# Performance work log

Measured on AMD Instinct MI355X. Metric: run time of the kernel, lower is better.

## Reference

```python
import jax, jax.numpy as jnp
import numpy as np

N_NODES = 32768
N_EDGES = 131072
BATCH = 512
SEQ_LEN = 1000
VOCAB = 26  # vocab_size=25 + 1 padding row
EMB = 128


def _bn(x, g, b):
    # BatchNorm1d forward with batch statistics (training-mode math), eps=1e-5
    m = x.mean(0)
    v = x.var(0)
    return g * (x - m) * jax.lax.rsqrt(v + 1e-5) + b


def _gcn(x, src, dst, W, b, n):
    deg = 1.0 + jax.ops.segment_sum(jnp.ones(src.shape[0], x.dtype), dst, num_segments=n)
    dis = jax.lax.rsqrt(deg)
    xw = x @ W
    msg = xw[src] * (dis[src] * dis[dst])[:, None]
    agg = jax.ops.segment_sum(msg, dst, num_segments=n) + xw * (dis * dis)[:, None]
    return agg + b


def _conv1d(x, k, b, pad):
    # x: [B, C_in, L], k: [C_out, C_in, K]
    y = jax.lax.conv_general_dilated(x, k, (1,), [(pad, pad)],
                                     dimension_numbers=('NCH', 'OIH', 'NCH'))
    return y + b[None, :, None]


def setup_inputs() -> dict:
    key = jax.random.key(0)
    ks = jax.random.split(key, 32)
    f = lambda i, shape, s=0.1: (jax.random.normal(ks[i], shape, dtype=jnp.float32) * s)
    inp = {
        'x': jax.random.normal(ks[0], (N_NODES, 5), dtype=jnp.float32),
        'edge_index': jax.random.randint(ks[1], (2, N_EDGES), 0, N_NODES, dtype=jnp.int32),
        'batch': jnp.sort(jax.random.randint(ks[2], (N_NODES,), 0, BATCH, dtype=jnp.int32)),
        'protein_seq': jax.random.randint(ks[3], (BATCH, SEQ_LEN), 0, VOCAB, dtype=jnp.int32),
        # GCN weights
        'W1': f(4, (5, 64)), 'b1': f(5, (64,)),
        'g1': jnp.ones((64,)), 'bt1': jnp.zeros((64,)),
        'W2': f(6, (64, 128)), 'b2': f(7, (128,)),
        'g2': jnp.ones((128,)), 'bt2': jnp.zeros((128,)),
        'W3': f(8, (128, 128)), 'b3': f(9, (128,)),
        'g3': jnp.ones((128,)), 'bt3': jnp.zeros((128,)),
        # protein embedding (row 0 = padding_idx, zeroed)
        'emb': f(10, (VOCAB, EMB)).at[0].set(0.0),
        # protein convs
        'ck1': f(11, (32, 128, 4)), 'cb1': f(12, (32,)),
        'ck2': f(13, (64, 32, 6)), 'cb2': f(14, (64,)),
        'ck3': f(15, (96, 64, 8)), 'cb3': f(16, (96,)),
        'fw1': f(17, (224, 512)), 'fb1': f(18, (512,)),
        'fw2': f(19, (512, 256)), 'fb2': f(20, (256,)),
        'fw3': f(21, (256, 1)), 'fb3': f(22, (1,)),
    }
    return inp


def reference(x, edge_index, batch, protein_seq,
              W1, b1, g1, bt1, W2, b2, g2, bt2, W3, b3, g3, bt3,
              emb, ck1, cb1, ck2, cb2, ck3, cb3,
              fw1, fb1, fw2, fb2, fw3, fb3):
    src, dst = edge_index[0], edge_index[1]
    relu = jax.nn.relu
    # Drug GNN encoder
    h = relu(_bn(_gcn(x, src, dst, W1, b1, N_NODES), g1, bt1))
    h = relu(_bn(_gcn(h, src, dst, W2, b2, N_NODES), g2, bt2))
    h = relu(_bn(_gcn(h, src, dst, W3, b3, N_NODES), g3, bt3))
    cnt = jax.ops.segment_sum(jnp.ones(N_NODES, h.dtype), batch, num_segments=BATCH)
    drug_emb = jax.ops.segment_sum(h, batch, num_segments=BATCH) / jnp.maximum(cnt, 1.0)[:, None]
    # Protein CNN encoder
    e = emb[protein_seq]                    # [B, L, 128]
    p = jnp.transpose(e, (0, 2, 1))         # [B, 128, L]
    p = relu(_conv1d(p, ck1, cb1, 1))       # [B, 32, 999]
    p = relu(_conv1d(p, ck2, cb2, 2))       # [B, 64, 998]
    p = relu(_conv1d(p, ck3, cb3, 3))       # [B, 96, 997]
    prot_emb = p.max(axis=2)                # [B, 96]
    c = jnp.concatenate([drug_emb, prot_emb], axis=1)  # [B, 224]
    c = relu(c @ fw1 + fb1)
    c = relu(c @ fw2 + fb2)
    out = (c @ fw3 + fb3)[:, 0]             # [B]
    return out
```

## Files before the change

### kernel.cpp

```cpp
#include <hip/hip_runtime.h>

#define NN 32768
#define NE 131072
#define NB 512
#define SL 1000

using bf16x8 = __attribute__((ext_vector_type(8))) short;
using f32x4  = __attribute__((ext_vector_type(4))) float;

static __device__ __forceinline__ unsigned short f2b(float f) {
  union { float f; unsigned u; } x; x.f = f;
  unsigned r = x.u + 0x7fffu + ((x.u >> 16) & 1u);
  return (unsigned short)(r >> 16);
}

static __device__ __forceinline__ void bn_from_raw(float sum, float ssq, float g, float b,
                                                   float& sc, float& sh) {
  float m = sum / 32768.f;
  float v = ssq / 32768.f - m * m;
  sc = g * rsqrtf(v + 1e-5f);
  sh = b - m * sc;
}

__global__ void k_degprep(const int* __restrict__ dst, int* __restrict__ degi,
                          const float* __restrict__ emb, const float* __restrict__ ck1,
                          const float* __restrict__ ck2, const float* __restrict__ ck3,
                          unsigned short* __restrict__ wt2, unsigned short* __restrict__ wt3,
                          float* __restrict__ e1) {
  int gid = blockIdx.x * 256 + threadIdx.x;
  atomicAdd(&degi[dst[gid]], 1);
  int idx = gid;
  if (idx < 12288) {
    int i = idx;
    int kt = i >> 11, co = (i >> 5) & 63, ci = i & 31;
    wt2[i] = f2b(ck2[co * 192 + ci * 6 + kt]);
  } else if (idx < 12288 + 49152) {
    int i = idx - 12288;
    int kt = i / 6144, co = (i >> 6) % 96, ci = i & 63;
    wt3[i] = f2b(ck3[co * 512 + ci * 8 + kt]);
  } else if (idx < 12288 + 49152 + 3328) {
    int i = idx - 61440;
    int t = i >> 7, kt = (i >> 5) & 3, co = i & 31;
    const float* er = emb + t * 128;
    float s = 0.f;
#pragma unroll 4
    for (int ci = 0; ci < 128; ++ci) s += er[ci] * ck1[co * 512 + ci * 4 + kt];
    e1[i] = s;
  }
}

__global__ void k_scan(const int* __restrict__ degi, int* __restrict__ base,
                       int* __restrict__ cursor, float* __restrict__ dis) {
  __shared__ int part[1024];
  int tid = threadIdx.x;
  int v[32];
  int s = 0;
  int lo = tid * 32;
#pragma unroll
  for (int i = 0; i < 32; ++i) { v[i] = degi[lo + i]; s += v[i]; }
  part[tid] = s;
  __syncthreads();
  for (int off = 1; off < 1024; off <<= 1) {
    int val = (tid >= off) ? part[tid - off] : 0;
    __syncthreads();
    part[tid] += val;
    __syncthreads();
  }
  int run = (tid > 0) ? part[tid - 1] : 0;
#pragma unroll
  for (int i = 0; i < 32; ++i) {
    base[lo + i] = run;
    cursor[lo + i] = run;
    dis[lo + i] = rsqrtf(1.0f + (float)v[i]);
    run += v[i];
  }
  if (tid == 1023) base[NN] = run;
}

__global__ void k_fill(const int* __restrict__ src, const int* __restrict__ dst,
                       int* __restrict__ cursor, unsigned short* __restrict__ csr_src,
                       const int* __restrict__ batch, int* __restrict__ blo,
                       int* __restrict__ bhi, int E) {
  int e = blockIdx.x * 256 + threadIdx.x;
  if (e < E) {
    int d = dst[e];
    int pos = atomicAdd(&cursor[d], 1);
    csr_src[pos] = (unsigned short)src[e];
  }
  if (e < NN) {
    int bb = batch[e];
    atomicMax(&bhi[bb], e + 1);
    atomicMax(&blo[bb], NN - e);
  }
}

__launch_bounds__(256)
__global__ void k_gfc1s(const float* __restrict__ x, const float* __restrict__ dis,
                        const int* __restrict__ base, const unsigned short* __restrict__ csr_src,
                        const float* __restrict__ W1, float* __restrict__ out,
                        float* __restrict__ st) {
  __shared__ float sW[5][64];
  __shared__ float a5[256][6];
  __shared__ float red[16][64];
  int tid = threadIdx.x;
  for (int i = tid; i < 320; i += 256) sW[i >> 6][i & 63] = W1[i];
  int n = blockIdx.x * 256 + tid;
  float dn = dis[n];
  float s2 = dn * dn;
  const float* xn = x + (long)n * 5;
  float a0 = xn[0] * s2, a1 = xn[1] * s2, a2 = xn[2] * s2, a3 = xn[3] * s2, a4 = xn[4] * s2;
  int b0 = base[n], b1 = base[n + 1];
  int sNext = (b0 < b1) ? csr_src[b0] : 0;
  for (int j = b0; j < b1; ++j) {
    int s = sNext;
    if (j + 1 < b1) sNext = csr_src[j + 1];
    float coef = dis[s] * dn;
    const float* xs = x + (long)s * 5;
    a0 += xs[0] * coef; a1 += xs[1] * coef; a2 += xs[2] * coef;
    a3 += xs[3] * coef; a4 += xs[4] * coef;
  }
  a5[tid][0] = a0; a5[tid][1] = a1; a5[tid][2] = a2; a5[tid][3] = a3; a5[tid][4] = a4;
  __syncthreads();
  int co = (tid & 15) * 4, strip = tid >> 4;
  float4 s4 = {0.f, 0.f, 0.f, 0.f}, ss4 = {0.f, 0.f, 0.f, 0.f};
  for (int i = 0; i < 16; ++i) {
    int nl = strip * 16 + i;
    long nn = (long)blockIdx.x * 256 + nl;
    float4 acc = {0.f, 0.f, 0.f, 0.f};
#pragma unroll
    for (int ci = 0; ci < 5; ++ci) {
      float av = a5[nl][ci];
      acc.x += av * sW[ci][co];     acc.y += av * sW[ci][co + 1];
      acc.z += av * sW[ci][co + 2]; acc.w += av * sW[ci][co + 3];
    }
    *(float4*)&out[nn * 64 + co] = acc;
    s4.x += acc.x; s4.y += acc.y; s4.z += acc.z; s4.w += acc.w;
    ss4.x += acc.x * acc.x; ss4.y += acc.y * acc.y;
    ss4.z += acc.z * acc.z; ss4.w += acc.w * acc.w;
  }
  *(float4*)&red[strip][co] = s4;
  __syncthreads();
  if (tid < 64) {
    float t = 0.f;
#pragma unroll
    for (int s = 0; s < 16; ++s) t += red[s][tid];
    atomicAdd(&st[tid], t);
  }
  __syncthreads();
  *(float4*)&red[strip][co] = ss4;
  __syncthreads();
  if (tid < 64) {
    float t = 0.f;
#pragma unroll
    for (int s = 0; s < 16; ++s) t += red[s][tid];
    atomicAdd(&st[64 + tid], t);
  }
}

template<int C>
__launch_bounds__(256)
__global__ void k_gbngather(const float* __restrict__ in, const float* __restrict__ dis,
                            const int* __restrict__ base, const unsigned short* __restrict__ csr_src,
                            const float* __restrict__ st, const float* __restrict__ g,
                            const float* __restrict__ bt, float* __restrict__ out) {
  constexpr int TPN = C / 4;
  int t = blockIdx.x * 256 + threadIdx.x;
  int n = t / TPN;
  int c = (t % TPN) * 4;
  float4 sum4 = *(const float4*)&st[c];
  float4 ssq4 = *(const float4*)&st[C + c];
  float4 gg = *(const float4*)&g[c];
  float4 bb = *(const float4*)&bt[c];
  float4 sc4, sh4;
  bn_from_raw(sum4.x, ssq4.x, gg.x, bb.x, sc4.x, sh4.x);
  bn_from_raw(sum4.y, ssq4.y, gg.y, bb.y, sc4.y, sh4.y);
  bn_from_raw(sum4.z, ssq4.z, gg.z, bb.z, sc4.z, sh4.z);
  bn_from_raw(sum4.w, ssq4.w, gg.w, bb.w, sc4.w, sh4.w);
  float dn = dis[n];
  float s2 = dn * dn;
  float4 a = *(const float4*)&in[(long)n * C + c];
  float4 acc;
  acc.x = fmaxf(a.x * sc4.x + sh4.x, 0.f) * s2;
  acc.y = fmaxf(a.y * sc4.y + sh4.y, 0.f) * s2;
  acc.z = fmaxf(a.z * sc4.z + sh4.z, 0.f) * s2;
  acc.w = fmaxf(a.w * sc4.w + sh4.w, 0.f) * s2;
  int b0 = base[n], b1 = base[n + 1];
  int sNext = (b0 < b1) ? csr_src[b0] : 0;
  for (int j = b0; j < b1; ++j) {
    int s = sNext;
    if (j + 1 < b1) sNext = csr_src[j + 1];
    float coef = dis[s] * dn;
    float4 vv = *(const float4*)&in[(long)s * C + c];
    acc.x += fmaxf(vv.x * sc4.x + sh4.x, 0.f) * coef;
    acc.y += fmaxf(vv.y * sc4.y + sh4.y, 0.f) * coef;
    acc.z += fmaxf(vv.z * sc4.z + sh4.z, 0.f) * coef;
    acc.w += fmaxf(vv.w * sc4.w + sh4.w, 0.f) * coef;
  }
  *(float4*)&out[(long)n * C + c] = acc;
}

template<int C_OUT, int K, int TN, bool RELU, bool BIAS, bool STATS>
__launch_bounds__(256)
__global__ void k_fc4(const float* __restrict__ in, const float* __restrict__ W,
                      const float* __restrict__ bias, float* __restrict__ out,
                      float* __restrict__ st, int N) {
  constexpr int CO4 = C_OUT / 4;
  constexpr int GPB = 256 / CO4;
  int g = blockIdx.x * GPB + threadIdx.x / CO4;
  long n0 = (long)g * TN;
  if (!STATS && n0 >= N) return;
  int co = (threadIdx.x % CO4) * 4;
  float4 acc[TN];
  float4 b4 = {0.f, 0.f, 0.f, 0.f};
  if (BIAS) b4 = *(const float4*)&bias[co];
#pragma unroll
  for (int t = 0; t < TN; ++t) acc[t] = b4;
  for (int ci = 0; ci < K; ci += 4) {
    float4 w0 = *(const float4*)&W[(long)(ci + 0) * C_OUT + co];
    float4 w1 = *(const float4*)&W[(long)(ci + 1) * C_OUT + co];
    float4 w2 = *(const float4*)&W[(long)(ci + 2) * C_OUT + co];
    float4 w3 = *(const float4*)&W[(long)(ci + 3) * C_OUT + co];
#pragma unroll
    for (int t = 0; t < TN; ++t) {
      float4 a = *(const float4*)&in[(n0 + t) * K + ci];
      acc[t].x += a.x * w0.x; acc[t].y += a.x * w0.y; acc[t].z += a.x * w0.z; acc[t].w += a.x * w0.w;
      acc[t].x += a.y * w1.x; acc[t].y += a.y * w1.y; acc[t].z += a.y * w1.z; acc[t].w += a.y * w1.w;
      acc[t].x += a.z * w2.x; acc[t].y += a.z * w2.y; acc[t].z += a.z * w2.z; acc[t].w += a.z * w2.w;
      acc[t].x += a.w * w3.x; acc[t].y += a.w * w3.y; acc[t].z += a.w * w3.z; acc[t].w += a.w * w3.w;
    }
  }
  float4 s4 = {0.f, 0.f, 0.f, 0.f}, ss4 = {0.f, 0.f, 0.f, 0.f};
#pragma unroll
  for (int t = 0; t < TN; ++t) {
    float4 o = acc[t];
    if (RELU) {
      o.x = fmaxf(o.x, 0.f); o.y = fmaxf(o.y, 0.f);
      o.z = fmaxf(o.z, 0.f); o.w = fmaxf(o.w, 0.f);
    }
    *(float4*)&out[(n0 + t) * C_OUT + co] = o;
    if (STATS) {
      s4.x += o.x; s4.y += o.y; s4.z += o.z; s4.w += o.w;
      ss4.x += o.x * o.x; ss4.y += o.y * o.y;
      ss4.z += o.z * o.z; ss4.w += o.w * o.w;
    }
  }
  if (STATS) {
    __shared__ float red2[GPB][C_OUT];
    int grp = threadIdx.x / CO4;
    *(float4*)&red2[grp][co] = s4;
    __syncthreads();
    if (threadIdx.x < C_OUT) {
      float t = 0.f;
#pragma unroll
      for (int s = 0; s < GPB; ++s) t += red2[s][threadIdx.x];
      atomicAdd(&st[threadIdx.x], t);
    }
    __syncthreads();
    *(float4*)&red2[grp][co] = ss4;
    __syncthreads();
    if (threadIdx.x < C_OUT) {
      float t = 0.f;
#pragma unroll
      for (int s = 0; s < GPB; ++s) t += red2[s][threadIdx.x];
      atomicAdd(&st[C_OUT + threadIdx.x], t);
    }
  }
}

__launch_bounds__(256)
__global__ void k_reg(const float* __restrict__ cbuf,
                      const int* __restrict__ blo, const int* __restrict__ bhi,
                      const float* __restrict__ agg, const float* __restrict__ st3,
                      const float* __restrict__ g3, const float* __restrict__ bt3,
                      const float* __restrict__ fw1, const float* __restrict__ fb1,
                      const float* __restrict__ fw2, const float* __restrict__ fb2,
                      const float* __restrict__ fw3, const float* __restrict__ fb3,
                      float* __restrict__ out) {
  __shared__ float cin[224];
  __shared__ float h1[512];
  __shared__ float h2[256];
  __shared__ float red[4];
  int b = blockIdx.x, t = threadIdx.x;
  if (t < 128) {
    int lo = NN - blo[b], hi = bhi[b];
    float sc, sh;
    bn_from_raw(st3[t], st3[128 + t], g3[t], bt3[t], sc, sh);
    float s = 0.f;
    for (int n = lo; n < hi; ++n) s += fmaxf(agg[(long)n * 128 + t] * sc + sh, 0.f);
    cin[t] = s / fmaxf((float)(hi - lo), 1.0f);
  } else if (t < 224) {
    cin[t] = cbuf[b * 224 + t];
  }
  __syncthreads();
  {
    float a0 = fb1[t], a1 = fb1[t + 256];
    for (int ci = 0; ci < 224; ++ci) {
      float av = cin[ci];
      a0 += av * fw1[ci * 512 + t];
      a1 += av * fw1[ci * 512 + t + 256];
    }
    h1[t] = fmaxf(a0, 0.f);
    h1[t + 256] = fmaxf(a1, 0.f);
  }
  __syncthreads();
  {
    float a = fb2[t];
    for (int ci = 0; ci < 512; ++ci) a += h1[ci] * fw2[ci * 256 + t];
    h2[t] = fmaxf(a, 0.f);
  }
  __syncthreads();
  {
    float p = h2[t] * fw3[t];
#pragma unroll
    for (int off = 32; off > 0; off >>= 1) p += __shfl_down(p, off, 64);
    if ((t & 63) == 0) red[t >> 6] = p;
    __syncthreads();
    if (t == 0) out[b] = red[0] + red[1] + red[2] + red[3] + fb3[0];
  }
}

__launch_bounds__(256, 3)
__global__ void conv_mfma(const int* __restrict__ seq, const float* __restrict__ e1g,
                          const float* __restrict__ cb1,
                          const unsigned short* __restrict__ wt2g, const float* __restrict__ cb2,
                          const unsigned short* __restrict__ wt3g, const float* __restrict__ cb3,
                          const float* __restrict__ gin, const float* __restrict__ dis,
                          const int* __restrict__ base, const unsigned short* __restrict__ csr_src,
                          const float* __restrict__ st2, const float* __restrict__ g2,
                          const float* __restrict__ bt2, float* __restrict__ gout,
                          float* __restrict__ outmax) {
  __shared__ __align__(16) unsigned short s_w[12288];
  __shared__ __align__(16) unsigned short s_c1[4864];
  __shared__ __align__(16) unsigned short s_c2[9216];
  __shared__ int s_tok[152];
  __shared__ int s_max[96];

  int tid = threadIdx.x;

  if (blockIdx.x >= 4096) {
    int t = (blockIdx.x - 4096) * 256 + tid;
    int n = t / 32;
    int c = (t % 32) * 4;
    float4 sum4 = *(const float4*)&st2[c];
    float4 ssq4 = *(const float4*)&st2[128 + c];
    float4 gg = *(const float4*)&g2[c];
    float4 bb = *(const float4*)&bt2[c];
    float4 sc4, sh4;
    bn_from_raw(sum4.x, ssq4.x, gg.x, bb.x, sc4.x, sh4.x);
    bn_from_raw(sum4.y, ssq4.y, gg.y, bb.y, sc4.y, sh4.y);
    bn_from_raw(sum4.z, ssq4.z, gg.z, bb.z, sc4.z, sh4.z);
    bn_from_raw(sum4.w, ssq4.w, gg.w, bb.w, sc4.w, sh4.w);
    float dn = dis[n];
    float s2 = dn * dn;
    float4 a = *(const float4*)&gin[(long)n * 128 + c];
    float4 acc;
    acc.x = fmaxf(a.x * sc4.x + sh4.x, 0.f) * s2;
    acc.y = fmaxf(a.y * sc4.y + sh4.y, 0.f) * s2;
    acc.z = fmaxf(a.z * sc4.z + sh4.z, 0.f) * s2;
    acc.w = fmaxf(a.w * sc4.w + sh4.w, 0.f) * s2;
    int b0 = base[n], b1 = base[n + 1];
    int sNext = (b0 < b1) ? csr_src[b0] : 0;
    for (int j = b0; j < b1; ++j) {
      int s = sNext;
      if (j + 1 < b1) sNext = csr_src[j + 1];
      float coef = dis[s] * dn;
      float4 vv = *(const float4*)&gin[(long)s * 128 + c];
      acc.x += fmaxf(vv.x * sc4.x + sh4.x, 0.f) * coef;
      acc.y += fmaxf(vv.y * sc4.y + sh4.y, 0.f) * coef;
      acc.z += fmaxf(vv.z * sc4.z + sh4.z, 0.f) * coef;
      acc.w += fmaxf(vv.w * sc4.w + sh4.w, 0.f) * coef;
    }
    *(float4*)&gout[(long)n * 128 + c] = acc;
    return;
  }

  int tile = blockIdx.x >> 9;
  int b = blockIdx.x & 511;
  int t0 = tile * 128;

  if (tid < 96) s_max[tid] = 0;
  if (tid < 152) {
    int p = t0 - 6 + tid;
    s_tok[tid] = (p >= 0 && p < SL) ? seq[b * SL + p] : 0;
  }
  if (tid < 128) ((int*)(s_c1 + 144 * 32))[tid] = 0;

  {
#pragma unroll
    for (int c = 0; c < 6; ++c) {
      int ch = c * 256 + tid;
      int row = ch >> 2;
      *(bf16x8*)&s_w[row * 32 + (((row ^ ch) & 3) << 3)] = *(const bf16x8*)(wt2g + ch * 8);
    }
  }
  __syncthreads();

  int lane = tid & 63, wave = tid >> 6;
  int l15 = lane & 15, quad = lane >> 4;

  {
    bool edge = (tile == 0) || (tile == 7);
#pragma unroll
    for (int pass = 0; pass < 2; ++pass) {
      int m = (pass == 0) ? (tid >> 1) : (128 + (tid >> 1));
      bool act = (pass == 0) || (tid < 32);
      if (act) {
        int co0 = (tid & 1) * 16;
        f32x4 a4[4];
#pragma unroll
        for (int q = 0; q < 4; ++q) a4[q] = *(const f32x4*)&cb1[co0 + q * 4];
#pragma unroll
        for (int kt = 0; kt < 4; ++kt) {
          const float* e = e1g + s_tok[m + kt] * 128 + kt * 32 + co0;
#pragma unroll
          for (int q = 0; q < 4; ++q) {
            f32x4 v = *(const f32x4*)&e[q * 4];
            a4[q][0] += v[0]; a4[q][1] += v[1]; a4[q][2] += v[2]; a4[q][3] += v[3];
          }
        }
        int l1 = t0 - 5 + m;
        bool ok = !edge || (l1 >= 0 && l1 < 999);
#pragma unroll
        for (int q = 0; q < 4; ++q) {
#pragma unroll
          for (int e2 = 0; e2 < 4; e2 += 2) {
            int co = co0 + q * 4 + e2;
            unsigned lo = ok ? (unsigned)f2b(fmaxf(a4[q][e2], 0.f)) : 0u;
            unsigned hi = ok ? (unsigned)f2b(fmaxf(a4[q][e2 + 1], 0.f)) : 0u;
            *(unsigned*)&s_c1[m * 32 + ((((co >> 3) ^ m) & 3) << 3) + (co & 7)] = lo | (hi << 16);
          }
        }
      }
    }
  }
  __syncthreads();

  {
    int mt0 = wave, mt1 = wave + 4;
    f32x4 acc[2][4];
#pragma unroll
    for (int nt = 0; nt < 4; ++nt) {
      float bv = cb2[nt * 16 + l15];
      acc[0][nt] = (f32x4){bv, bv, bv, bv};
      acc[1][nt] = (f32x4){bv, bv, bv, bv};
    }
    for (int kt = 0; kt < 6; ++kt) {
      int r0 = mt0 * 16 + l15 + kt, r1 = mt1 * 16 + l15 + kt;
      bf16x8 a0 = *(const bf16x8*)&s_c1[r0 * 32 + (((quad ^ r0) & 3) << 3)];
      bf16x8 a1 = *(const bf16x8*)&s_c1[r1 * 32 + (((quad ^ r1) & 3) << 3)];
#pragma unroll
      for (int nt = 0; nt < 4; ++nt) {
        int wr = kt * 64 + nt * 16 + l15;
        bf16x8 bf = *(const bf16x8*)&s_w[wr * 32 + (((quad ^ wr) & 3) << 3)];
        acc[0][nt] = __builtin_amdgcn_mfma_f32_16x16x32_bf16(a0, bf, acc[0][nt], 0, 0, 0);
        acc[1][nt] = __builtin_amdgcn_mfma_f32_16x16x32_bf16(a1, bf, acc[1][nt], 0, 0, 0);
      }
    }
#pragma unroll
    for (int mb = 0; mb < 2; ++mb) {
      int mt = mb ? mt1 : mt0;
#pragma unroll
      for (int nt = 0; nt < 4; ++nt) {
        int co = nt * 16 + l15;
#pragma unroll
        for (int r = 0; r < 4; ++r) {
          int m = mt * 16 + quad * 4 + r;
          int l2 = t0 - 3 + m;
          unsigned short hv = f2b(fmaxf(acc[mb][nt][r], 0.f));
          s_c2[m * 64 + ((((co >> 3) ^ m) & 7) << 3) + (co & 7)] = (l2 >= 0 && l2 < 998) ? hv : (unsigned short)0;
        }
      }
    }
    if (wave == 0) {
      f32x4 acc8[4];
#pragma unroll
      for (int nt = 0; nt < 4; ++nt) {
        float bv = cb2[nt * 16 + l15];
        acc8[nt] = (f32x4){bv, bv, bv, bv};
      }
      for (int kt = 0; kt < 6; ++kt) {
        int r0 = 128 + l15 + kt;
        bf16x8 a0 = *(const bf16x8*)&s_c1[r0 * 32 + (((quad ^ r0) & 3) << 3)];
#pragma unroll
        for (int nt = 0; nt < 4; ++nt) {
          int wr = kt * 64 + nt * 16 + l15;
          bf16x8 bf = *(const bf16x8*)&s_w[wr * 32 + (((quad ^ wr) & 3) << 3)];
          acc8[nt] = __builtin_amdgcn_mfma_f32_16x16x32_bf16(a0, bf, acc8[nt], 0, 0, 0);
        }
      }
#pragma unroll
      for (int nt = 0; nt < 4; ++nt) {
        int co = nt * 16 + l15;
#pragma unroll
        for (int r = 0; r < 4; ++r) {
          int m = 128 + quad * 4 + r;
          int l2 = t0 - 3 + m;
          unsigned short hv = f2b(fmaxf(acc8[nt][r], 0.f));
          s_c2[m * 64 + ((((co >> 3) ^ m) & 7) << 3) + (co & 7)] = (l2 >= 0 && l2 < 998) ? hv : (unsigned short)0;
        }
      }
    }
  }

  {
    bf16x8 w3t[3];
#pragma unroll
    for (int c = 0; c < 3; ++c) w3t[c] = *(const bf16x8*)(wt3g + (c * 256 + tid) * 8);
    __syncthreads();
#pragma unroll
    for (int c = 0; c < 3; ++c) {
      int ch = c * 256 + tid;
      int row = ch >> 3;
      *(bf16x8*)&s_w[row * 64 + (((row ^ ch) & 7) << 3)] = w3t[c];
    }
    __syncthreads();
  }

  {
    int mt0 = wave, mt1 = wave + 4;
    f32x4 acc[2][6];
#pragma unroll
    for (int nt = 0; nt < 6; ++nt) {
      float bv = cb3[nt * 16 + l15];
      acc[0][nt] = (f32x4){bv, bv, bv, bv};
      acc[1][nt] = (f32x4){bv, bv, bv, bv};
    }
    for (int kt = 0; kt < 8; ++kt) {
      bf16x8 w3t[3];
      if (kt < 7) {
#pragma unroll
        for (int c = 0; c < 3; ++c)
          w3t[c] = *(const bf16x8*)(wt3g + ((kt + 1) * 768 + c * 256 + tid) * 8);
      }
      int bo = (kt & 1) * 6144;
      int ra0 = mt0 * 16 + l15 + kt, ra1 = mt1 * 16 + l15 + kt;
#pragma unroll
      for (int cb = 0; cb < 2; ++cb) {
        bf16x8 a0 = *(const bf16x8*)&s_c2[ra0 * 64 + ((((cb * 4 + quad) ^ ra0) & 7) << 3)];
        bf16x8 a1 = *(const bf16x8*)&s_c2[ra1 * 64 + ((((cb * 4 + quad) ^ ra1) & 7) << 3)];
#pragma unroll
        for (int nt = 0; nt < 6; ++nt) {
          int wr = nt * 16 + l15;
          bf16x8 bf = *(const bf16x8*)&s_w[bo + wr * 64 + ((((cb * 4 + quad) ^ wr) & 7) << 3)];
          acc[0][nt] = __builtin_amdgcn_mfma_f32_16x16x32_bf16(a0, bf, acc[0][nt], 0, 0, 0);
          acc[1][nt] = __builtin_amdgcn_mfma_f32_16x16x32_bf16(a1, bf, acc[1][nt], 0, 0, 0);
        }
      }
      if (kt < 7) {
        int bo2 = 6144 - bo;
#pragma unroll
        for (int c = 0; c < 3; ++c) {
          int ch = c * 256 + tid;
          int row = ch >> 3;
          *(bf16x8*)&s_w[bo2 + row * 64 + (((row ^ ch) & 7) << 3)] = w3t[c];
        }
      }
      __syncthreads();
    }
#pragma unroll
    for (int nt = 0; nt < 6; ++nt) {
      int co = nt * 16 + l15;
      float mx = 0.f;
#pragma unroll
      for (int mb = 0; mb < 2; ++mb) {
        int mt = mb ? mt1 : mt0;
#pragma unroll
        for (int r = 0; r < 4; ++r) {
          int l3 = t0 + mt * 16 + quad * 4 + r;
          if (l3 < 997) mx = fmaxf(mx, acc[mb][nt][r]);
        }
      }
      atomicMax(&s_max[co], __float_as_int(mx));
    }
  }
  __syncthreads();
  if (tid < 96) atomicMax((int*)&outmax[b * 224 + 128 + tid], s_max[tid]);
}

extern "C" void kernel_launch(void* const* d_in, const int* in_sizes, int n_in,
                              void* d_out, int out_size, void* d_ws, size_t ws_size,
                              hipStream_t stream) {
  (void)in_sizes; (void)n_in; (void)out_size; (void)ws_size;
  const float* x = (const float*)d_in[0];
  const int* ei = (const int*)d_in[1];
  const int* batch = (const int*)d_in[2];
  const int* seq = (const int*)d_in[3];
  const float* W1 = (const float*)d_in[4];
  const float* g1 = (const float*)d_in[6];
  const float* bt1 = (const float*)d_in[7];
  const float* W2 = (const float*)d_in[8];
  const float* g2 = (const float*)d_in[10];
  const float* bt2 = (const float*)d_in[11];
  const float* W3 = (const float*)d_in[12];
  const float* g3 = (const float*)d_in[14];
  const float* bt3 = (const float*)d_in[15];
  const float* emb = (const float*)d_in[16];
  const float* ck1 = (const float*)d_in[17];
  const float* cb1 = (const float*)d_in[18];
  const float* ck2 = (const float*)d_in[19];
  const float* cb2 = (const float*)d_in[20];
  const float* ck3 = (const float*)d_in[21];
  const float* cb3 = (const float*)d_in[22];
  const float* fw1 = (const float*)d_in[23];
  const float* fb1 = (const float*)d_in[24];
  const float* fw2 = (const float*)d_in[25];
  const float* fb2 = (const float*)d_in[26];
  const float* fw3 = (const float*)d_in[27];
  const float* fb3 = (const float*)d_in[28];
  const int* src = ei;
  const int* dst = ei + NE;

  float* ws = (float*)d_ws;
  float* bufA = ws;
  float* bufB = ws + 4194304;
  float* dis = ws + 8388608;
  float* stats = ws + 8421376;
  float* cbuf = ws + 8422032;
  int* degi = (int*)(ws + 8536720);
  int* base = degi + NN;
  int* cursor = base + NN + 1;
  unsigned short* csr_src = (unsigned short*)(cursor + NN);
  unsigned short* emb_bf = (unsigned short*)(ws + 8700564);
  unsigned short* wt1 = emb_bf + 3328;
  unsigned short* wt2 = wt1 + 16384;
  unsigned short* wt3 = wt2 + 12288;
  float* e1 = ws + 8741140;
  int* blo = (int*)(ws + 8744468);
  int* bhi = blo + 512;
  float* out = (float*)d_out;

  hipMemsetAsync(stats, 0, (656 + 114688 + 32768) * sizeof(float), stream);
  hipMemsetAsync(blo, 0, 1024 * sizeof(int), stream);

  k_degprep<<<NE / 256, 256, 0, stream>>>(dst, degi, emb, ck1, ck2, ck3, wt2, wt3, e1);
  k_scan<<<1, 1024, 0, stream>>>(degi, base, cursor, dis);
  k_fill<<<NE / 256, 256, 0, stream>>>(src, dst, cursor, csr_src, batch, blo, bhi, NE);

  k_gfc1s<<<NN / 256, 256, 0, stream>>>(x, dis, base, csr_src, W1, bufA, stats);
  k_gbngather<64><<<NN * 16 / 256, 256, 0, stream>>>(bufA, dis, base, csr_src, stats, g1, bt1, bufB);
  k_fc4<128, 64, 4, false, false, true><<<1024, 256, 0, stream>>>(bufB, W2, nullptr, bufA, stats + 128, NN);

  conv_mfma<<<8192, 256, 0, stream>>>(seq, e1, cb1, wt2, cb2, wt3, cb3,
                                      bufA, dis, base, csr_src, stats + 128, g2, bt2, bufB,
                                      cbuf);

  k_fc4<128, 128, 4, false, false, true><<<1024, 256, 0, stream>>>(bufB, W3, nullptr, bufA, stats + 384, NN);

  k_reg<<<NB, 256, 0, stream>>>(cbuf, blo, bhi, bufA, stats + 384, g3, bt3,
                                fw1, fb1, fw2, fb2, fw3, fb3, out);
}
```

Before: 429.1 us.

## Split first GCN layer and mean-pool into finer-grained kernels, drop atomic batch bounds

The first-layer aggregate plus FC plus stats kernel is split in two. A 64-thread-block gather writes 5-wide aggregates to a buffer, and a separate kernel does the 5x64 projection with one node per 16-thread group to raise block count. Graph segment bounds are now found by binary search over the sorted batch array in a new pooling kernel instead of atomicMax in k_fill, which also removes a memset. Mean pooling moves out of the regressor into its own kernel. The cost is extra launches and an intermediate round trip through global memory.

```diff
diff --git a/kernel.cpp b/kernel.cpp
--- a/kernel.cpp
+++ b/kernel.cpp
@@ -78,33 +78,20 @@
 }
 
 __global__ void k_fill(const int* __restrict__ src, const int* __restrict__ dst,
-                       int* __restrict__ cursor, unsigned short* __restrict__ csr_src,
-                       const int* __restrict__ batch, int* __restrict__ blo,
-                       int* __restrict__ bhi, int E) {
+                       int* __restrict__ cursor, unsigned short* __restrict__ csr_src, int E) {
   int e = blockIdx.x * 256 + threadIdx.x;
   if (e < E) {
     int d = dst[e];
     int pos = atomicAdd(&cursor[d], 1);
     csr_src[pos] = (unsigned short)src[e];
   }
-  if (e < NN) {
-    int bb = batch[e];
-    atomicMax(&bhi[bb], e + 1);
-    atomicMax(&blo[bb], NN - e);
-  }
-}
-
-__launch_bounds__(256)
-__global__ void k_gfc1s(const float* __restrict__ x, const float* __restrict__ dis,
-                        const int* __restrict__ base, const unsigned short* __restrict__ csr_src,
-                        const float* __restrict__ W1, float* __restrict__ out,
-                        float* __restrict__ st) {
-  __shared__ float sW[5][64];
-  __shared__ float a5[256][6];
-  __shared__ float red[16][64];
-  int tid = threadIdx.x;
-  for (int i = tid; i < 320; i += 256) sW[i >> 6][i & 63] = W1[i];
-  int n = blockIdx.x * 256 + tid;
+}
+
+__launch_bounds__(64)
+__global__ void k_agg5(const float* __restrict__ x, const float* __restrict__ dis,
+                       const int* __restrict__ base, const unsigned short* __restrict__ csr_src,
+                       float* __restrict__ a5g) {
+  int n = blockIdx.x * 64 + threadIdx.x;
   float dn = dis[n];
   float s2 = dn * dn;
   const float* xn = x + (long)n * 5;
@@ -119,26 +106,33 @@
     a0 += xs[0] * coef; a1 += xs[1] * coef; a2 += xs[2] * coef;
     a3 += xs[3] * coef; a4 += xs[4] * coef;
   }
-  a5[tid][0] = a0; a5[tid][1] = a1; a5[tid][2] = a2; a5[tid][3] = a3; a5[tid][4] = a4;
-  __syncthreads();
-  int co = (tid & 15) * 4, strip = tid >> 4;
-  float4 s4 = {0.f, 0.f, 0.f, 0.f}, ss4 = {0.f, 0.f, 0.f, 0.f};
-  for (int i = 0; i < 16; ++i) {
-    int nl = strip * 16 + i;
-    long nn = (long)blockIdx.x * 256 + nl;
-    float4 acc = {0.f, 0.f, 0.f, 0.f};
-#pragma unroll
-    for (int ci = 0; ci < 5; ++ci) {
-      float av = a5[nl][ci];
-      acc.x += av * sW[ci][co];     acc.y += av * sW[ci][co + 1];
-      acc.z += av * sW[ci][co + 2]; acc.w += av * sW[ci][co + 3];
-    }
-    *(float4*)&out[nn * 64 + co] = acc;
-    s4.x += acc.x; s4.y += acc.y; s4.z += acc.z; s4.w += acc.w;
-    ss4.x += acc.x * acc.x; ss4.y += acc.y * acc.y;
-    ss4.z += acc.z * acc.z; ss4.w += acc.w * acc.w;
-  }
-  *(float4*)&red[strip][co] = s4;
+  float* o = a5g + (long)n * 5;
+  o[0] = a0; o[1] = a1; o[2] = a2; o[3] = a3; o[4] = a4;
+}
+
+__launch_bounds__(256)
+__global__ void k_fc5s(const float* __restrict__ a5g, const float* __restrict__ W1,
+                       float* __restrict__ out, float* __restrict__ st) {
+  __shared__ float sW[5][64];
+  __shared__ float red[16][64];
+  int tid = threadIdx.x;
+  for (int i = tid; i < 320; i += 256) sW[i >> 6][i & 63] = W1[i];
+  __syncthreads();
+  int grp = tid >> 4;
+  int co = (tid & 15) * 4;
+  long n = (long)blockIdx.x * 16 + grp;
+  float a[5];
+#pragma unroll
+  for (int ci = 0; ci < 5; ++ci) a[ci] = a5g[n * 5 + ci];
+  float4 acc = {0.f, 0.f, 0.f, 0.f};
+#pragma unroll
+  for (int ci = 0; ci < 5; ++ci) {
+    float av = a[ci];
+    acc.x += av * sW[ci][co];     acc.y += av * sW[ci][co + 1];
+    acc.z += av * sW[ci][co + 2]; acc.w += av * sW[ci][co + 3];
+  }
+  *(float4*)&out[n * 64 + co] = acc;
+  *(float4*)&red[grp][co] = acc;
   __syncthreads();
   if (tid < 64) {
     float t = 0.f;
@@ -147,7 +141,9 @@
     atomicAdd(&st[tid], t);
   }
   __syncthreads();
-  *(float4*)&red[strip][co] = ss4;
+  float4 ss;
+  ss.x = acc.x * acc.x; ss.y = acc.y * acc.y; ss.z = acc.z * acc.z; ss.w = acc.w * acc.w;
+  *(float4*)&red[grp][co] = ss;
   __syncthreads();
   if (tid < 64) {
     float t = 0.f;
@@ -267,11 +263,33 @@
   }
 }
 
+__launch_bounds__(128)
+__global__ void k_pool(const float* __restrict__ agg, const float* __restrict__ st3,
+                       const float* __restrict__ g3, const float* __restrict__ bt3,
+                       const int* __restrict__ batch, float* __restrict__ outmax) {
+  __shared__ int s_lo, s_hi;
+  int b = blockIdx.x, tid = threadIdx.x;
+  if (tid == 0) {
+    int lo = 0, hi = NN;
+    while (lo < hi) { int m = (lo + hi) >> 1; if (batch[m] < b) lo = m + 1; else hi = m; }
+    s_lo = lo;
+    hi = NN;
+    while (lo < hi) { int m = (lo + hi) >> 1; if (batch[m] <= b) lo = m + 1; else hi = m; }
+    s_hi = lo;
+  }
+  __syncthreads();
+  {
+    int lo = s_lo, hi = s_hi, c = tid;
+    float sc, sh;
+    bn_from_raw(st3[c], st3[128 + c], g3[c], bt3[c], sc, sh);
+    float s = 0.f;
+    for (int n = lo; n < hi; ++n) s += fmaxf(agg[(long)n * 128 + c] * sc + sh, 0.f);
+    outmax[b * 224 + c] = s / fmaxf((float)(hi - lo), 1.0f);
+  }
+}
+
 __launch_bounds__(256)
 __global__ void k_reg(const float* __restrict__ cbuf,
-                      const int* __restrict__ blo, const int* __restrict__ bhi,
-                      const float* __restrict__ agg, const float* __restrict__ st3,
-                      const float* __restrict__ g3, const float* __restrict__ bt3,
                       const float* __restrict__ fw1, const float* __restrict__ fb1,
                       const float* __restrict__ fw2, const float* __restrict__ fb2,
                       const float* __restrict__ fw3, const float* __restrict__ fb3,
@@ -281,16 +299,7 @@
   __shared__ float h2[256];
   __shared__ float red[4];
   int b = blockIdx.x, t = threadIdx.x;
-  if (t < 128) {
-    int lo = NN - blo[b], hi = bhi[b];
-    float sc, sh;
-    bn_from_raw(st3[t], st3[128 + t], g3[t], bt3[t], sc, sh);
-    float s = 0.f;
-    for (int n = lo; n < hi; ++n) s += fmaxf(agg[(long)n * 128 + t] * sc + sh, 0.f);
-    cin[t] = s / fmaxf((float)(hi - lo), 1.0f);
-  } else if (t < 224) {
-    cin[t] = cbuf[b * 224 + t];
-  }
+  if (t < 224) cin[t] = cbuf[b * 224 + t];
   __syncthreads();
   {
     float a0 = fb1[t], a1 = fb1[t + 256];
@@ -625,18 +634,17 @@
   unsigned short* wt2 = wt1 + 16384;
   unsigned short* wt3 = wt2 + 12288;
   float* e1 = ws + 8741140;
-  int* blo = (int*)(ws + 8744468);
-  int* bhi = blo + 512;
+  float* a5g = bufB;
   float* out = (float*)d_out;
 
   hipMemsetAsync(stats, 0, (656 + 114688 + 32768) * sizeof(float), stream);
-  hipMemsetAsync(blo, 0, 1024 * sizeof(int), stream);
 
   k_degprep<<<NE / 256, 256, 0, stream>>>(dst, degi, emb, ck1, ck2, ck3, wt2, wt3, e1);
   k_scan<<<1, 1024, 0, stream>>>(degi, base, cursor, dis);
-  k_fill<<<NE / 256, 256, 0, stream>>>(src, dst, cursor, csr_src, batch, blo, bhi, NE);
-
-  k_gfc1s<<<NN / 256, 256, 0, stream>>>(x, dis, base, csr_src, W1, bufA, stats);
+  k_fill<<<NE / 256, 256, 0, stream>>>(src, dst, cursor, csr_src, NE);
+
+  k_agg5<<<NN / 64, 64, 0, stream>>>(x, dis, base, csr_src, a5g);
+  k_fc5s<<<NN / 16, 256, 0, stream>>>(a5g, W1, bufA, stats);
   k_gbngather<64><<<NN * 16 / 256, 256, 0, stream>>>(bufA, dis, base, csr_src, stats, g1, bt1, bufB);
   k_fc4<128, 64, 4, false, false, true><<<1024, 256, 0, stream>>>(bufB, W2, nullptr, bufA, stats + 128, NN);
 
@@ -646,6 +654,6 @@
 
   k_fc4<128, 128, 4, false, false, true><<<1024, 256, 0, stream>>>(bufB, W3, nullptr, bufA, stats + 384, NN);
 
-  k_reg<<<NB, 256, 0, stream>>>(cbuf, blo, bhi, bufA, stats + 384, g3, bt3,
-                                fw1, fb1, fw2, fb2, fw3, fb3, out);
-}
+  k_pool<<<NB, 128, 0, stream>>>(bufA, stats + 384, g3, bt3, batch, cbuf);
+  k_reg<<<NB, 256, 0, stream>>>(cbuf, fw1, fb1, fw2, fb2, fw3, fb3, out);
+}
```

Result: slower. 466.0 us (+8.6%).

## Split graph mean-pooling into a separate 4-way chunked kernel with binary-search bounds

Applied to the files above, without the earlier changes.

Moves the per-graph BN+ReLU+mean pooling out of the regressor kernel into a new kernel that splits each graph's node range into four chunks across blocks, writing partial sums that the regressor then adds up. Graph boundaries are found by binary search over the sorted batch array instead of atomicMax in the CSR fill kernel, which drops a memset and the atomics. The goal is more parallelism for the serial per-graph node loop. The cost is an extra kernel launch and a round trip of the partial sums through global memory.

```diff
diff --git a/kernel.cpp b/kernel.cpp
--- a/kernel.cpp
+++ b/kernel.cpp
@@ -78,19 +78,12 @@
 }
 
 __global__ void k_fill(const int* __restrict__ src, const int* __restrict__ dst,
-                       int* __restrict__ cursor, unsigned short* __restrict__ csr_src,
-                       const int* __restrict__ batch, int* __restrict__ blo,
-                       int* __restrict__ bhi, int E) {
+                       int* __restrict__ cursor, unsigned short* __restrict__ csr_src, int E) {
   int e = blockIdx.x * 256 + threadIdx.x;
   if (e < E) {
     int d = dst[e];
     int pos = atomicAdd(&cursor[d], 1);
     csr_src[pos] = (unsigned short)src[e];
-  }
-  if (e < NN) {
-    int bb = batch[e];
-    atomicMax(&bhi[bb], e + 1);
-    atomicMax(&blo[bb], NN - e);
   }
 }
 
@@ -267,11 +260,35 @@
   }
 }
 
+__launch_bounds__(128)
+__global__ void k_pool4(const float* __restrict__ agg, const float* __restrict__ st3,
+                        const float* __restrict__ g3, const float* __restrict__ bt3,
+                        const int* __restrict__ batch, float* __restrict__ part) {
+  __shared__ int s_lo, s_hi;
+  int b = blockIdx.x, chunk = blockIdx.y, tid = threadIdx.x;
+  if (tid == 0) {
+    int lo = 0, hi = NN;
+    while (lo < hi) { int m = (lo + hi) >> 1; if (batch[m] < b) lo = m + 1; else hi = m; }
+    s_lo = lo;
+    hi = NN;
+    while (lo < hi) { int m = (lo + hi) >> 1; if (batch[m] <= b) lo = m + 1; else hi = m; }
+    s_hi = lo;
+  }
+  __syncthreads();
+  int lo = s_lo, hi = s_hi;
+  int q = (hi - lo + 3) >> 2;
+  int st = lo + chunk * q;
+  int en = min(st + q, hi);
+  float sc, sh;
+  bn_from_raw(st3[tid], st3[128 + tid], g3[tid], bt3[tid], sc, sh);
+  float s = 0.f;
+  for (int n = st; n < en; ++n) s += fmaxf(agg[(long)n * 128 + tid] * sc + sh, 0.f);
+  part[b * 512 + chunk * 128 + tid] = s;
+  if (chunk == 0 && tid == 0) part[262144 + b] = (float)(hi - lo);
+}
+
 __launch_bounds__(256)
-__global__ void k_reg(const float* __restrict__ cbuf,
-                      const int* __restrict__ blo, const int* __restrict__ bhi,
-                      const float* __restrict__ agg, const float* __restrict__ st3,
-                      const float* __restrict__ g3, const float* __restrict__ bt3,
+__global__ void k_reg(const float* __restrict__ cbuf, const float* __restrict__ part,
                       const float* __restrict__ fw1, const float* __restrict__ fb1,
                       const float* __restrict__ fw2, const float* __restrict__ fb2,
                       const float* __restrict__ fw3, const float* __restrict__ fb3,
@@ -282,12 +299,9 @@
   __shared__ float red[4];
   int b = blockIdx.x, t = threadIdx.x;
   if (t < 128) {
-    int lo = NN - blo[b], hi = bhi[b];
-    float sc, sh;
-    bn_from_raw(st3[t], st3[128 + t], g3[t], bt3[t], sc, sh);
-    float s = 0.f;
-    for (int n = lo; n < hi; ++n) s += fmaxf(agg[(long)n * 128 + t] * sc + sh, 0.f);
-    cin[t] = s / fmaxf((float)(hi - lo), 1.0f);
+    float cnt = fmaxf(part[262144 + b], 1.0f);
+    cin[t] = (part[b * 512 + t] + part[b * 512 + 128 + t] +
+              part[b * 512 + 256 + t] + part[b * 512 + 384 + t]) / cnt;
   } else if (t < 224) {
     cin[t] = cbuf[b * 224 + t];
   }
@@ -625,16 +639,13 @@
   unsigned short* wt2 = wt1 + 16384;
   unsigned short* wt3 = wt2 + 12288;
   float* e1 = ws + 8741140;
-  int* blo = (int*)(ws + 8744468);
-  int* bhi = blo + 512;
   float* out = (float*)d_out;
 
   hipMemsetAsync(stats, 0, (656 + 114688 + 32768) * sizeof(float), stream);
-  hipMemsetAsync(blo, 0, 1024 * sizeof(int), stream);
 
   k_degprep<<<NE / 256, 256, 0, stream>>>(dst, degi, emb, ck1, ck2, ck3, wt2, wt3, e1);
   k_scan<<<1, 1024, 0, stream>>>(degi, base, cursor, dis);
-  k_fill<<<NE / 256, 256, 0, stream>>>(src, dst, cursor, csr_src, batch, blo, bhi, NE);
+  k_fill<<<NE / 256, 256, 0, stream>>>(src, dst, cursor, csr_src, NE);
 
   k_gfc1s<<<NN / 256, 256, 0, stream>>>(x, dis, base, csr_src, W1, bufA, stats);
   k_gbngather<64><<<NN * 16 / 256, 256, 0, stream>>>(bufA, dis, base, csr_src, stats, g1, bt1, bufB);
@@ -646,6 +657,6 @@
 
   k_fc4<128, 128, 4, false, false, true><<<1024, 256, 0, stream>>>(bufB, W3, nullptr, bufA, stats + 384, NN);
 
-  k_reg<<<NB, 256, 0, stream>>>(cbuf, blo, bhi, bufA, stats + 384, g3, bt3,
-                                fw1, fb1, fw2, fb2, fw3, fb3, out);
-}
+  k_pool4<<<dim3(NB, 4), 128, 0, stream>>>(bufA, stats + 384, g3, bt3, batch, bufB);
+  k_reg<<<NB, 256, 0, stream>>>(cbuf, bufB, fw1, fb1, fw2, fb2, fw3, fb3, out);
+}
```

Measured after the change: 407.3 us (median of 2 runs). 1.05x faster.
